# Kernel optimization log

Measured on AMD Instinct MI355X. Metric: run time of the kernel, lower is better.

## Reference

```python
import jax, jax.numpy as jnp
import numpy as np

B, DIM, T = 8, 1024, 4096
CB, CD = 4096, 8          # codebook_size, codebook_dim
COMMIT = 0.25
EPS = 1e-12


def _weight_norm(v, g):
    # torch weight_norm over dim=0: per-output-channel norm of v
    n = jnp.sqrt(jnp.sum(v * v, axis=1, keepdims=True))
    return g[:, None] * v / n


def _l2_normalize(x):
    n = jnp.sqrt(jnp.sum(x * x, axis=1, keepdims=True))
    return x / jnp.maximum(n, EPS)


def setup_inputs() -> dict:
    key = jax.random.key(0)
    ks = jax.random.split(key, 5)
    z = jax.random.normal(ks[0], (B, DIM, T), jnp.float32)
    v_in = jax.random.normal(ks[1], (CD, DIM), jnp.float32) * 0.02   # conv1d k=1 weight (squeezed)
    g_in = jnp.sqrt(jnp.sum(v_in * v_in, axis=1))                     # weight_norm init: g = ||v||
    b_in = jnp.zeros((CD,), jnp.float32)
    codebook = jax.random.normal(ks[2], (CB, CD), jnp.float32)        # nn.Embedding default N(0,1)
    v_out = jax.random.normal(ks[3], (DIM, CD), jnp.float32) * 0.02
    g_out = jnp.sqrt(jnp.sum(v_out * v_out, axis=1))
    b_out = jnp.zeros((DIM,), jnp.float32)
    return {"z": z, "v_in": v_in, "g_in": g_in, "b_in": b_in,
            "codebook": codebook, "v_out": v_out, "g_out": g_out, "b_out": b_out}


def reference(z, v_in, g_in, b_in, codebook, v_out, g_out, b_out):
    # in_proj: weight-normed 1x1 Conv1d == per-timestep matmul
    W_in = _weight_norm(v_in, g_in)                              # [CD, DIM]
    z_e = jnp.einsum('od,bdt->bot', W_in, z) + b_in[None, :, None]  # [B, CD, T]

    # decode_latents: normalize encodings and codebook, squared-L2 distances
    enc = z_e.transpose(0, 2, 1).reshape(B * T, CD)              # (b t) d
    e_n = _l2_normalize(enc)                                     # [BT, CD]
    c_n = _l2_normalize(codebook)                                # [CB, CD]
    dist = (jnp.sum(e_n * e_n, axis=1, keepdims=True)
            - 2.0 * (e_n @ c_n.T)
            + jnp.sum(c_n * c_n, axis=1)[None, :])               # [BT, CB]
    indices = jnp.argmin(dist, axis=1).reshape(B, T)             # [B, T] int

    # decode_code: gather UN-normalized codebook, transpose to [B, CD, T]
    z_q = codebook[indices].transpose(0, 2, 1)                   # [B, CD, T]

    # training losses (per-batch), commitment + codebook
    sg = jax.lax.stop_gradient
    commitment_loss = jnp.mean((z_e - sg(z_q)) ** 2, axis=(1, 2)) * COMMIT
    codebook_loss = jnp.mean((z_q - sg(z_e)) ** 2, axis=(1, 2))
    commit_loss = commitment_loss + codebook_loss                # [B]

    # straight-through estimator
    z_q_ste = z_e + sg(z_q - z_e)                                # [B, CD, T]

    # out_proj
    W_out = _weight_norm(v_out, g_out)                           # [DIM, CD]
    out = jnp.einsum('oc,bct->bot', W_out, z_q_ste) + b_out[None, :, None]  # [B, DIM, T]
    return out, indices, commit_loss
```

## Files before the change

### kernel.cpp

```cpp
#include <hip/hip_runtime.h>

#define DIMN 1024
#define TN 4096
#define BN 8
#define CBN 4096
#define CDN 8
#define BTN (BN*TN)
#define OUT_ELEMS (BN*DIMN*TN)

typedef float fx4 __attribute__((ext_vector_type(4)));
typedef float fx2 __attribute__((ext_vector_type(2)));

#define WS_WINT 0
#define WS_WOUT 8192
#define WS_CN   16384
#define WS_C2   49152
#define WS_LOSS 86016
#define WS_CNT  86024

#define LBO_F   8256
#define LZEP_F  9296
#define LZE_F   13648
#define LEN_F   14160
#define LCAND_F 14672
#define LZQ_F   15184
#define LDS_TOT 15696

__device__ __forceinline__ float dot4(float4 a, float4 b) {
    float d = a.x * b.x;
    d = fmaf(a.y, b.y, d);
    d = fmaf(a.z, b.z, d);
    d = fmaf(a.w, b.w, d);
    return d;
}
__device__ __forceinline__ void add4(float4& a, float4 b) {
    a.x += b.x; a.y += b.y; a.z += b.z; a.w += b.w;
}

__global__ __launch_bounds__(256) void k0_prep(
    const float* __restrict__ v_in, const float* __restrict__ g_in,
    const float* __restrict__ codebook, const float* __restrict__ v_out,
    const float* __restrict__ g_out, float* __restrict__ ws) {
    __shared__ float sred[5];
    int blk = blockIdx.x, tid = threadIdx.x;
    if (blk < 8) {
        int o = blk;
        const float* v = v_in + o * DIMN;
        float4 x = *(const float4*)(v + tid * 4);
        float p = x.x * x.x + x.y * x.y + x.z * x.z + x.w * x.w;
        for (int off = 32; off >= 1; off >>= 1) p += __shfl_down(p, off, 64);
        if ((tid & 63) == 0) sred[tid >> 6] = p;
        __syncthreads();
        if (tid == 0) {
            float tot = sred[0] + sred[1] + sred[2] + sred[3];
            sred[4] = g_in[o] / sqrtf(tot);
        }
        __syncthreads();
        float s = sred[4];
        ws[WS_WINT + (tid * 4 + 0) * 8 + o] = x.x * s;
        ws[WS_WINT + (tid * 4 + 1) * 8 + o] = x.y * s;
        ws[WS_WINT + (tid * 4 + 2) * 8 + o] = x.z * s;
        ws[WS_WINT + (tid * 4 + 3) * 8 + o] = x.w * s;
    } else if (blk < 12) {
        int r = (blk - 8) * 256 + tid;
        const float* v = v_out + r * 8;
        float4 a = *(const float4*)v;
        float4 b = *(const float4*)(v + 4);
        float n2 = dot4(a, a) + dot4(b, b);
        float s = g_out[r] / sqrtf(n2);
        *(float4*)(ws + WS_WOUT + r * 8)     = make_float4(a.x*s, a.y*s, a.z*s, a.w*s);
        *(float4*)(ws + WS_WOUT + r * 8 + 4) = make_float4(b.x*s, b.y*s, b.z*s, b.w*s);
    } else if (blk < 28) {
        int j = (blk - 12) * 256 + tid;
        const float* c = codebook + j * 8;
        float4 a = *(const float4*)c;
        float4 b = *(const float4*)(c + 4);
        float n2 = dot4(a, a) + dot4(b, b);
        float inv = 1.0f / fmaxf(sqrtf(n2), 1e-12f);
        float4 na = make_float4(a.x*inv, a.y*inv, a.z*inv, a.w*inv);
        float4 nb = make_float4(b.x*inv, b.y*inv, b.z*inv, b.w*inv);
        *(float4*)(ws + WS_CN + j * 8)     = na;
        *(float4*)(ws + WS_CN + j * 8 + 4) = nb;
        ws[WS_C2 + j] = -0.5f * (dot4(na, na) + dot4(nb, nb));
    } else {
        if (tid < 9) ws[WS_LOSS + tid] = 0.0f;
    }
}

__global__ __launch_bounds__(256, 2) void k_mega(
    const float* __restrict__ z, const float* __restrict__ b_in,
    const float* __restrict__ codebook, const float* __restrict__ b_out,
    float* __restrict__ dout, float* __restrict__ ws) {
    __shared__ float sp[LDS_TOT];
    int tid = threadIdx.x, blk = blockIdx.x;
    int b = blk >> 6;
    int t0 = (blk & 63) * 64;

    #pragma unroll
    for (int i = 0; i < 8; i++) {
        int f4 = tid + i * 256;
        *(float4*)(sp + f4 * 4) = *(const float4*)(ws + WS_WINT + f4 * 4);
    }
    __syncthreads();
    {
        int p = tid >> 5, tpair = tid & 31;
        int tA = tpair * 2;
        const float* zp = z + ((size_t)(b * DIMN + p * 128)) * TN + t0 + tA;
        float4 a0a = make_float4(0.f,0.f,0.f,0.f), a0b = make_float4(0.f,0.f,0.f,0.f);
        float4 a1a = make_float4(0.f,0.f,0.f,0.f), a1b = make_float4(0.f,0.f,0.f,0.f);
        #pragma unroll 8
        for (int dd = 0; dd < 128; ++dd) {
            fx2 zv = __builtin_nontemporal_load((const fx2*)(zp + (size_t)dd * TN));
            const float* wv = sp + (p * 128 + dd) * 8;
            float4 w0 = *(const float4*)wv;
            float4 w1 = *(const float4*)(wv + 4);
            a0a.x = fmaf(w0.x, zv.x, a0a.x); a0a.y = fmaf(w0.y, zv.x, a0a.y);
            a0a.z = fmaf(w0.z, zv.x, a0a.z); a0a.w = fmaf(w0.w, zv.x, a0a.w);
            a0b.x = fmaf(w1.x, zv.x, a0b.x); a0b.y = fmaf(w1.y, zv.x, a0b.y);
            a0b.z = fmaf(w1.z, zv.x, a0b.z); a0b.w = fmaf(w1.w, zv.x, a0b.w);
            a1a.x = fmaf(w0.x, zv.y, a1a.x); a1a.y = fmaf(w0.y, zv.y, a1a.y);
            a1a.z = fmaf(w0.z, zv.y, a1a.z); a1a.w = fmaf(w0.w, zv.y, a1a.w);
            a1b.x = fmaf(w1.x, zv.y, a1b.x); a1b.y = fmaf(w1.y, zv.y, a1b.y);
            a1b.z = fmaf(w1.z, zv.y, a1b.z); a1b.w = fmaf(w1.w, zv.y, a1b.w);
        }
        float* q0 = sp + LZEP_F + tA * 68 + p * 8;
        *(float4*)(q0)     = a0a;
        *(float4*)(q0 + 4) = a0b;
        float* q1 = sp + LZEP_F + (tA + 1) * 68 + p * 8;
        *(float4*)(q1)     = a1a;
        *(float4*)(q1 + 4) = a1b;
    }
    __syncthreads();

    if (tid < 64) {
        int t = tid;
        float4 za = *(const float4*)(b_in);
        float4 zb = *(const float4*)(b_in + 4);
        #pragma unroll
        for (int p = 0; p < 8; p++) {
            const float* pp = sp + LZEP_F + t * 68 + p * 8;
            add4(za, *(const float4*)(pp));
            add4(zb, *(const float4*)(pp + 4));
        }
        *(float4*)(sp + LZE_F + t * 8)     = za;
        *(float4*)(sp + LZE_F + t * 8 + 4) = zb;
        float inv = 1.0f / fmaxf(sqrtf(dot4(za, za) + dot4(zb, zb)), 1e-12f);
        *(float4*)(sp + LEN_F + t * 8)     = make_float4(za.x*inv, za.y*inv, za.z*inv, za.w*inv);
        *(float4*)(sp + LEN_F + t * 8 + 4) = make_float4(zb.x*inv, zb.y*inv, zb.z*inv, zb.w*inv);
    }
    __syncthreads();

    int co = tid >> 3, tt = tid & 7;
    float en[8][8];
    #pragma unroll
    for (int k = 0; k < 8; k++) {
        float4 u = *(const float4*)(sp + LEN_F + (tt * 8 + k) * 8);
        float4 v = *(const float4*)(sp + LEN_F + (tt * 8 + k) * 8 + 4);
        en[k][0]=u.x; en[k][1]=u.y; en[k][2]=u.z; en[k][3]=u.w;
        en[k][4]=v.x; en[k][5]=v.y; en[k][6]=v.z; en[k][7]=v.w;
    }
    float bs[8]; int bj[8];
    #pragma unroll
    for (int k = 0; k < 8; k++) { bs[k] = -3.4e38f; bj[k] = 0; }
    #pragma unroll 1
    for (int ci = 0; ci < 16; ++ci) {
        int j0 = ci * 256 + co * 8;
        #pragma unroll
        for (int qh = 0; qh < 2; ++qh) {
            int jq = j0 + qh * 4;
            const float* cg = ws + WS_CN + (size_t)jq * 8;
            float4 ca[4], cb[4];
            #pragma unroll
            for (int k = 0; k < 4; k++) {
                ca[k] = *(const float4*)(cg + k * 8);
                cb[k] = *(const float4*)(cg + k * 8 + 4);
            }
            float4 hqv = *(const float4*)(ws + WS_C2 + jq);
            float hv[4] = {hqv.x, hqv.y, hqv.z, hqv.w};
            #pragma unroll
            for (int k = 0; k < 4; k++) {
                #pragma unroll
                for (int t = 0; t < 8; t++) {
                    float s = fmaf(en[t][0], ca[k].x, hv[k]);
                    s = fmaf(en[t][1], ca[k].y, s); s = fmaf(en[t][2], ca[k].z, s);
                    s = fmaf(en[t][3], ca[k].w, s);
                    s = fmaf(en[t][4], cb[k].x, s); s = fmaf(en[t][5], cb[k].y, s);
                    s = fmaf(en[t][6], cb[k].z, s); s = fmaf(en[t][7], cb[k].w, s);
                    if (s > bs[t]) { bs[t] = s; bj[t] = jq + k; }
                }
            }
        }
    }
    #pragma unroll
    for (int st = 8; st <= 32; st <<= 1) {
        #pragma unroll
        for (int t = 0; t < 8; t++) {
            float os = __shfl_xor(bs[t], st, 64);
            int   oj = __shfl_xor(bj[t], st, 64);
            if (os > bs[t] || (os == bs[t] && oj < bj[t])) { bs[t] = os; bj[t] = oj; }
        }
    }
    if ((tid & 63) < 8) {
        int w = tid >> 6;
        #pragma unroll
        for (int k = 0; k < 8; k++)
            *(float2*)(sp + LCAND_F + (w * 64 + tt * 8 + k) * 2) =
                make_float2(bs[k], __int_as_float(bj[k]));
    }
    __syncthreads();

    if (tid < 64) {
        int t = tid;
        float2 c0 = *(const float2*)(sp + LCAND_F + t * 2);
        float best = c0.x; int idx = __float_as_int(c0.y);
        #pragma unroll
        for (int w2 = 1; w2 < 4; w2++) {
            float2 cw = *(const float2*)(sp + LCAND_F + (w2 * 64 + t) * 2);
            int j2 = __float_as_int(cw.y);
            if (cw.x > best || (cw.x == best && j2 < idx)) { best = cw.x; idx = j2; }
        }
        dout[(size_t)OUT_ELEMS + b * TN + t0 + t] = (float)idx;
        const float* cq = codebook + (size_t)idx * 8;
        float4 qa = *(const float4*)cq, qb = *(const float4*)(cq + 4);
        sp[LZQ_F + 0*64 + t] = qa.x; sp[LZQ_F + 1*64 + t] = qa.y;
        sp[LZQ_F + 2*64 + t] = qa.z; sp[LZQ_F + 3*64 + t] = qa.w;
        sp[LZQ_F + 4*64 + t] = qb.x; sp[LZQ_F + 5*64 + t] = qb.y;
        sp[LZQ_F + 6*64 + t] = qb.z; sp[LZQ_F + 7*64 + t] = qb.w;
        float4 za = *(const float4*)(sp + LZE_F + t * 8);
        float4 zb = *(const float4*)(sp + LZE_F + t * 8 + 4);
        float4 da = make_float4(za.x-qa.x, za.y-qa.y, za.z-qa.z, za.w-qa.w);
        float4 db = make_float4(zb.x-qb.x, zb.y-qb.y, zb.z-qb.z, zb.w-qb.w);
        float l = dot4(da, da) + dot4(db, db);
        for (int off = 32; off >= 1; off >>= 1) l += __shfl_down(l, off, 64);
        if (t == 0) atomicAdd(ws + WS_LOSS + b, l);
    } else {
        int i = tid - 64;
        #pragma unroll
        for (int r = 0; r < 11; r++) {
            int f4 = r * 192 + i;
            if (f4 < 2048) {
                float4 v = *(const float4*)(ws + WS_WOUT + f4 * 4);
                *(float4*)(sp + f4 * 4 + 4 * (f4 >> 7)) = v;
            }
        }
        #pragma unroll
        for (int r = 0; r < 2; r++) {
            int f = r * 192 + i;
            if (f < 256) {
                float4 v = *(const float4*)(b_out + f * 4);
                int sk = f >> 4;
                sp[LBO_F + f * 4 + sk + 0] = v.x;
                sp[LBO_F + f * 4 + sk + 1] = v.y;
                sp[LBO_F + f * 4 + sk + 2] = v.z;
                sp[LBO_F + f * 4 + sk + 3] = v.w;
            }
        }
    }
    __syncthreads();

    int t4 = tid & 15, og = tid >> 4;
    float4 zr[8];
    #pragma unroll
    for (int c = 0; c < 8; c++) zr[c] = *(const float4*)(sp + LZQ_F + c * 64 + t4 * 4);
    size_t obase = ((size_t)(b * DIMN + og * 64)) * TN + (size_t)(t0 + t4 * 4);
    for (int k = 0; k < 64; k++) {
        int o = og * 64 + k;
        const float* wrow = sp + o * 8 + 4 * og;
        float4 wa = *(const float4*)(wrow);
        float4 wb = *(const float4*)(wrow + 4);
        float bo = sp[LBO_F + o + og];
        float4 acc = make_float4(bo, bo, bo, bo);
        float wc[8] = {wa.x, wa.y, wa.z, wa.w, wb.x, wb.y, wb.z, wb.w};
        #pragma unroll
        for (int c = 0; c < 8; c++) {
            acc.x = fmaf(wc[c], zr[c].x, acc.x);
            acc.y = fmaf(wc[c], zr[c].y, acc.y);
            acc.z = fmaf(wc[c], zr[c].z, acc.z);
            acc.w = fmaf(wc[c], zr[c].w, acc.w);
        }
        acc.x = fminf(fmaxf(acc.x, -8.f), 8.f);
        acc.y = fminf(fmaxf(acc.y, -8.f), 8.f);
        acc.z = fminf(fmaxf(acc.z, -8.f), 8.f);
        acc.w = fminf(fmaxf(acc.w, -8.f), 8.f);
        fx4 st; st.x = acc.x; st.y = acc.y; st.z = acc.z; st.w = acc.w;
        __builtin_nontemporal_store(st, (fx4*)(dout + obase + (size_t)k * TN));
    }

    if (tid == 0) {
        __threadfence();
        unsigned int old = atomicAdd((unsigned int*)(ws + WS_CNT), 1u);
        if (old == 511u) {
            #pragma unroll
            for (int i = 0; i < 8; i++) {
                float v = atomicAdd(ws + WS_LOSS + i, 0.0f);
                dout[(size_t)OUT_ELEMS + BTN + i] = v * (1.25f / 32768.0f);
            }
        }
    }
}

extern "C" void kernel_launch(void* const* d_in, const int* in_sizes, int n_in,
                              void* d_out, int out_size, void* d_ws, size_t ws_size,
                              hipStream_t stream) {
    (void)in_sizes; (void)n_in; (void)out_size; (void)ws_size;
    const float* z        = (const float*)d_in[0];
    const float* v_in     = (const float*)d_in[1];
    const float* g_in     = (const float*)d_in[2];
    const float* b_in     = (const float*)d_in[3];
    const float* codebook = (const float*)d_in[4];
    const float* v_out    = (const float*)d_in[5];
    const float* g_out    = (const float*)d_in[6];
    const float* b_out    = (const float*)d_in[7];
    float* out            = (float*)d_out;
    float* ws             = (float*)d_ws;

    hipLaunchKernelGGL(k0_prep, dim3(29), dim3(256), 0, stream,
                       v_in, g_in, codebook, v_out, g_out, ws);
    hipLaunchKernelGGL(k_mega, dim3(512), dim3(256), 0, stream,
                       z, b_in, codebook, b_out, out, ws);
}
```

Before: 294.9 us.

## Use packed FP32 FMAs, 512-thread blocks and pair-interleaved codebook layout

After: 297.6 us. About the same (+0.9%).

```diff
diff --git a/kernel.cpp b/kernel.cpp
--- a/kernel.cpp
+++ b/kernel.cpp
@@ -4,7 +4,6 @@
 #define TN 4096
 #define BN 8
 #define CBN 4096
-#define CDN 8
 #define BTN (BN*TN)
 #define OUT_ELEMS (BN*DIMN*TN)
 
@@ -13,18 +12,15 @@
 
 #define WS_WINT 0
 #define WS_WOUT 8192
-#define WS_CN   16384
 #define WS_C2   49152
+#define WS_CNP  53248
 #define WS_LOSS 86016
 #define WS_CNT  86024
 
-#define LBO_F   8256
-#define LZEP_F  9296
-#define LZE_F   13648
-#define LEN_F   14160
-#define LCAND_F 14672
-#define LZQ_F   15184
-#define LDS_TOT 15696
+#define LROWS_F 8192
+#define LROW    68
+#define LZQ_F   12544
+#define LDS_TOT 13056
 
 __device__ __forceinline__ float dot4(float4 a, float4 b) {
     float d = a.x * b.x;
@@ -36,6 +32,13 @@
 __device__ __forceinline__ void add4(float4& a, float4 b) {
     a.x += b.x; a.y += b.y; a.z += b.z; a.w += b.w;
 }
+__device__ __forceinline__ fx2 lo2(fx4 v) { return __builtin_shufflevector(v, v, 0, 1); }
+__device__ __forceinline__ fx2 hi2(fx4 v) { return __builtin_shufflevector(v, v, 2, 3); }
+__device__ __forceinline__ fx2 splat2(float x) { fx2 r; r.x = x; r.y = x; return r; }
+__device__ __forceinline__ fx2 fma2(fx2 a, fx2 b, fx2 c) { return __builtin_elementwise_fma(a, b, c); }
+__device__ __forceinline__ fx2 max2(fx2 a, fx2 b) { return __builtin_elementwise_max(a, b); }
+__device__ __forceinline__ fx2 min2(fx2 a, fx2 b) { return __builtin_elementwise_min(a, b); }
+__device__ __forceinline__ fx4 cat4(fx2 a, fx2 b) { return __builtin_shufflevector(a, b, 0, 1, 2, 3); }
 
 __global__ __launch_bounds__(256) void k0_prep(
     const float* __restrict__ v_in, const float* __restrict__ g_in,
@@ -77,17 +80,21 @@
         float4 b = *(const float4*)(c + 4);
         float n2 = dot4(a, a) + dot4(b, b);
         float inv = 1.0f / fmaxf(sqrtf(n2), 1e-12f);
-        float4 na = make_float4(a.x*inv, a.y*inv, a.z*inv, a.w*inv);
-        float4 nb = make_float4(b.x*inv, b.y*inv, b.z*inv, b.w*inv);
-        *(float4*)(ws + WS_CN + j * 8)     = na;
-        *(float4*)(ws + WS_CN + j * 8 + 4) = nb;
-        ws[WS_C2 + j] = -0.5f * (dot4(na, na) + dot4(nb, nb));
+        float na[8] = {a.x*inv, a.y*inv, a.z*inv, a.w*inv,
+                       b.x*inv, b.y*inv, b.z*inv, b.w*inv};
+        float* dst = ws + WS_CNP + (size_t)(j >> 1) * 16 + (j & 1);
+        #pragma unroll
+        for (int i = 0; i < 8; i++) dst[i * 2] = na[i];
+        float h = 0.0f;
+        #pragma unroll
+        for (int i = 0; i < 8; i++) h = fmaf(na[i], na[i], h);
+        ws[WS_C2 + j] = -0.5f * h;
     } else {
         if (tid < 9) ws[WS_LOSS + tid] = 0.0f;
     }
 }
 
-__global__ __launch_bounds__(256, 2) void k_mega(
+__global__ __launch_bounds__(512, 4) void k_mega(
     const float* __restrict__ z, const float* __restrict__ b_in,
     const float* __restrict__ codebook, const float* __restrict__ b_out,
     float* __restrict__ dout, float* __restrict__ ws) {
@@ -97,38 +104,36 @@
     int t0 = (blk & 63) * 64;
 
     #pragma unroll
-    for (int i = 0; i < 8; i++) {
-        int f4 = tid + i * 256;
-        *(float4*)(sp + f4 * 4) = *(const float4*)(ws + WS_WINT + f4 * 4);
-    }
-    __syncthreads();
-    {
+    for (int i = 0; i < 4; i++) {
+        int f4 = tid + i * 512;
+        *(fx4*)(sp + f4 * 4) = *(const fx4*)(ws + WS_WINT + f4 * 4);
+    }
+    __syncthreads();
+
+    if (tid < 256) {
         int p = tid >> 5, tpair = tid & 31;
         int tA = tpair * 2;
         const float* zp = z + ((size_t)(b * DIMN + p * 128)) * TN + t0 + tA;
-        float4 a0a = make_float4(0.f,0.f,0.f,0.f), a0b = make_float4(0.f,0.f,0.f,0.f);
-        float4 a1a = make_float4(0.f,0.f,0.f,0.f), a1b = make_float4(0.f,0.f,0.f,0.f);
+        fx2 a0aL = splat2(0.f), a0aH = splat2(0.f), a0bL = splat2(0.f), a0bH = splat2(0.f);
+        fx2 a1aL = splat2(0.f), a1aH = splat2(0.f), a1bL = splat2(0.f), a1bH = splat2(0.f);
         #pragma unroll 8
         for (int dd = 0; dd < 128; ++dd) {
             fx2 zv = __builtin_nontemporal_load((const fx2*)(zp + (size_t)dd * TN));
             const float* wv = sp + (p * 128 + dd) * 8;
-            float4 w0 = *(const float4*)wv;
-            float4 w1 = *(const float4*)(wv + 4);
-            a0a.x = fmaf(w0.x, zv.x, a0a.x); a0a.y = fmaf(w0.y, zv.x, a0a.y);
-            a0a.z = fmaf(w0.z, zv.x, a0a.z); a0a.w = fmaf(w0.w, zv.x, a0a.w);
-            a0b.x = fmaf(w1.x, zv.x, a0b.x); a0b.y = fmaf(w1.y, zv.x, a0b.y);
-            a0b.z = fmaf(w1.z, zv.x, a0b.z); a0b.w = fmaf(w1.w, zv.x, a0b.w);
-            a1a.x = fmaf(w0.x, zv.y, a1a.x); a1a.y = fmaf(w0.y, zv.y, a1a.y);
-            a1a.z = fmaf(w0.z, zv.y, a1a.z); a1a.w = fmaf(w0.w, zv.y, a1a.w);
-            a1b.x = fmaf(w1.x, zv.y, a1b.x); a1b.y = fmaf(w1.y, zv.y, a1b.y);
-            a1b.z = fmaf(w1.z, zv.y, a1b.z); a1b.w = fmaf(w1.w, zv.y, a1b.w);
-        }
-        float* q0 = sp + LZEP_F + tA * 68 + p * 8;
-        *(float4*)(q0)     = a0a;
-        *(float4*)(q0 + 4) = a0b;
-        float* q1 = sp + LZEP_F + (tA + 1) * 68 + p * 8;
-        *(float4*)(q1)     = a1a;
-        *(float4*)(q1 + 4) = a1b;
+            fx4 w0 = *(const fx4*)wv;
+            fx4 w1 = *(const fx4*)(wv + 4);
+            fx2 zx = splat2(zv.x), zy = splat2(zv.y);
+            a0aL = fma2(lo2(w0), zx, a0aL); a0aH = fma2(hi2(w0), zx, a0aH);
+            a0bL = fma2(lo2(w1), zx, a0bL); a0bH = fma2(hi2(w1), zx, a0bH);
+            a1aL = fma2(lo2(w0), zy, a1aL); a1aH = fma2(hi2(w0), zy, a1aH);
+            a1bL = fma2(lo2(w1), zy, a1bL); a1bH = fma2(hi2(w1), zy, a1bH);
+        }
+        float* q0 = sp + LROWS_F + tA * LROW + p * 8;
+        *(fx4*)(q0)     = cat4(a0aL, a0aH);
+        *(fx4*)(q0 + 4) = cat4(a0bL, a0bH);
+        float* q1 = sp + LROWS_F + (tA + 1) * LROW + p * 8;
+        *(fx4*)(q1)     = cat4(a1aL, a1aH);
+        *(fx4*)(q1 + 4) = cat4(a1bL, a1bH);
     }
     __syncthreads();
 
@@ -138,84 +143,97 @@
         float4 zb = *(const float4*)(b_in + 4);
         #pragma unroll
         for (int p = 0; p < 8; p++) {
-            const float* pp = sp + LZEP_F + t * 68 + p * 8;
+            const float* pp = sp + LROWS_F + t * LROW + p * 8;
             add4(za, *(const float4*)(pp));
             add4(zb, *(const float4*)(pp + 4));
         }
-        *(float4*)(sp + LZE_F + t * 8)     = za;
-        *(float4*)(sp + LZE_F + t * 8 + 4) = zb;
+        float* row = sp + LROWS_F + t * LROW;
+        *(float4*)(row)     = za;
+        *(float4*)(row + 4) = zb;
         float inv = 1.0f / fmaxf(sqrtf(dot4(za, za) + dot4(zb, zb)), 1e-12f);
-        *(float4*)(sp + LEN_F + t * 8)     = make_float4(za.x*inv, za.y*inv, za.z*inv, za.w*inv);
-        *(float4*)(sp + LEN_F + t * 8 + 4) = make_float4(zb.x*inv, zb.y*inv, zb.z*inv, zb.w*inv);
-    }
-    __syncthreads();
-
-    int co = tid >> 3, tt = tid & 7;
-    float en[8][8];
-    #pragma unroll
-    for (int k = 0; k < 8; k++) {
-        float4 u = *(const float4*)(sp + LEN_F + (tt * 8 + k) * 8);
-        float4 v = *(const float4*)(sp + LEN_F + (tt * 8 + k) * 8 + 4);
+        *(float4*)(row + 8)  = make_float4(za.x*inv, za.y*inv, za.z*inv, za.w*inv);
+        *(float4*)(row + 12) = make_float4(zb.x*inv, zb.y*inv, zb.z*inv, zb.w*inv);
+    }
+    __syncthreads();
+
+    int co = tid >> 4, tg = tid & 15;
+    float en[4][8];
+    #pragma unroll
+    for (int k = 0; k < 4; k++) {
+        const float* rp = sp + LROWS_F + (tg * 4 + k) * LROW + 8;
+        fx4 u = *(const fx4*)rp;
+        fx4 v = *(const fx4*)(rp + 4);
         en[k][0]=u.x; en[k][1]=u.y; en[k][2]=u.z; en[k][3]=u.w;
         en[k][4]=v.x; en[k][5]=v.y; en[k][6]=v.z; en[k][7]=v.w;
     }
-    float bs[8]; int bj[8];
-    #pragma unroll
-    for (int k = 0; k < 8; k++) { bs[k] = -3.4e38f; bj[k] = 0; }
+    fx2 bs[4]; int bje[4], bjo[4];
+    #pragma unroll
+    for (int k = 0; k < 4; k++) { bs[k] = splat2(-3.4e38f); bje[k] = 0; bjo[k] = 1; }
     #pragma unroll 1
     for (int ci = 0; ci < 16; ++ci) {
         int j0 = ci * 256 + co * 8;
-        #pragma unroll
-        for (int qh = 0; qh < 2; ++qh) {
-            int jq = j0 + qh * 4;
-            const float* cg = ws + WS_CN + (size_t)jq * 8;
-            float4 ca[4], cb[4];
+        const float* cg = ws + WS_CNP + (size_t)j0 * 8;
+        #pragma unroll
+        for (int pp = 0; pp < 4; ++pp) {
+            fx4 cA = *(const fx4*)(cg + pp * 16);
+            fx4 cB = *(const fx4*)(cg + pp * 16 + 4);
+            fx4 cC = *(const fx4*)(cg + pp * 16 + 8);
+            fx4 cD = *(const fx4*)(cg + pp * 16 + 12);
+            fx2 h2 = *(const fx2*)(ws + WS_C2 + j0 + pp * 2);
+            int jE = j0 + pp * 2;
             #pragma unroll
             for (int k = 0; k < 4; k++) {
-                ca[k] = *(const float4*)(cg + k * 8);
-                cb[k] = *(const float4*)(cg + k * 8 + 4);
+                fx2 s = h2;
+                s = fma2(splat2(en[k][0]), lo2(cA), s);
+                s = fma2(splat2(en[k][1]), hi2(cA), s);
+                s = fma2(splat2(en[k][2]), lo2(cB), s);
+                s = fma2(splat2(en[k][3]), hi2(cB), s);
+                s = fma2(splat2(en[k][4]), lo2(cC), s);
+                s = fma2(splat2(en[k][5]), hi2(cC), s);
+                s = fma2(splat2(en[k][6]), lo2(cD), s);
+                s = fma2(splat2(en[k][7]), hi2(cD), s);
+                bool cE = s.x > bs[k].x;
+                bool cO = s.y > bs[k].y;
+                bs[k] = max2(bs[k], s);
+                if (cE) bje[k] = jE;
+                if (cO) bjo[k] = jE + 1;
             }
-            float4 hqv = *(const float4*)(ws + WS_C2 + jq);
-            float hv[4] = {hqv.x, hqv.y, hqv.z, hqv.w};
-            #pragma unroll
-            for (int k = 0; k < 4; k++) {
-                #pragma unroll
-                for (int t = 0; t < 8; t++) {
-                    float s = fmaf(en[t][0], ca[k].x, hv[k]);
-                    s = fmaf(en[t][1], ca[k].y, s); s = fmaf(en[t][2], ca[k].z, s);
-                    s = fmaf(en[t][3], ca[k].w, s);
-                    s = fmaf(en[t][4], cb[k].x, s); s = fmaf(en[t][5], cb[k].y, s);
-                    s = fmaf(en[t][6], cb[k].z, s); s = fmaf(en[t][7], cb[k].w, s);
-                    if (s > bs[t]) { bs[t] = s; bj[t] = jq + k; }
-                }
-            }
-        }
-    }
-    #pragma unroll
-    for (int st = 8; st <= 32; st <<= 1) {
-        #pragma unroll
-        for (int t = 0; t < 8; t++) {
-            float os = __shfl_xor(bs[t], st, 64);
-            int   oj = __shfl_xor(bj[t], st, 64);
-            if (os > bs[t] || (os == bs[t] && oj < bj[t])) { bs[t] = os; bj[t] = oj; }
-        }
-    }
-    if ((tid & 63) < 8) {
+        }
+    }
+    float bsF[4]; int bjF[4];
+    #pragma unroll
+    for (int k = 0; k < 4; k++) {
+        bsF[k] = bs[k].x; bjF[k] = bje[k];
+        if (bs[k].y > bsF[k] || (bs[k].y == bsF[k] && bjo[k] < bjF[k])) {
+            bsF[k] = bs[k].y; bjF[k] = bjo[k];
+        }
+    }
+    #pragma unroll
+    for (int st = 16; st <= 32; st <<= 1) {
+        #pragma unroll
+        for (int k = 0; k < 4; k++) {
+            float os = __shfl_xor(bsF[k], st, 64);
+            int   oj = __shfl_xor(bjF[k], st, 64);
+            if (os > bsF[k] || (os == bsF[k] && oj < bjF[k])) { bsF[k] = os; bjF[k] = oj; }
+        }
+    }
+    if ((tid & 63) < 16) {
         int w = tid >> 6;
         #pragma unroll
-        for (int k = 0; k < 8; k++)
-            *(float2*)(sp + LCAND_F + (w * 64 + tt * 8 + k) * 2) =
-                make_float2(bs[k], __int_as_float(bj[k]));
+        for (int k = 0; k < 4; k++)
+            *(fx2*)(sp + LROWS_F + (tg * 4 + k) * LROW + 32 + w * 2) =
+                (fx2){bsF[k], __int_as_float(bjF[k])};
     }
     __syncthreads();
 
     if (tid < 64) {
         int t = tid;
-        float2 c0 = *(const float2*)(sp + LCAND_F + t * 2);
+        const float* crow = sp + LROWS_F + t * LROW + 32;
+        fx2 c0 = *(const fx2*)(crow);
         float best = c0.x; int idx = __float_as_int(c0.y);
         #pragma unroll
-        for (int w2 = 1; w2 < 4; w2++) {
-            float2 cw = *(const float2*)(sp + LCAND_F + (w2 * 64 + t) * 2);
+        for (int w2 = 1; w2 < 8; w2++) {
+            fx2 cw = *(const fx2*)(crow + w2 * 2);
             int j2 = __float_as_int(cw.y);
             if (cw.x > best || (cw.x == best && j2 < idx)) { best = cw.x; idx = j2; }
         }
@@ -226,8 +244,9 @@
         sp[LZQ_F + 2*64 + t] = qa.z; sp[LZQ_F + 3*64 + t] = qa.w;
         sp[LZQ_F + 4*64 + t] = qb.x; sp[LZQ_F + 5*64 + t] = qb.y;
         sp[LZQ_F + 6*64 + t] = qb.z; sp[LZQ_F + 7*64 + t] = qb.w;
-        float4 za = *(const float4*)(sp + LZE_F + t * 8);
-        float4 zb = *(const float4*)(sp + LZE_F + t * 8 + 4);
+        const float* row = sp + LROWS_F + t * LROW;
+        float4 za = *(const float4*)(row);
+        float4 zb = *(const float4*)(row + 4);
         float4 da = make_float4(za.x-qa.x, za.y-qa.y, za.z-qa.z, za.w-qa.w);
         float4 db = make_float4(zb.x-qb.x, zb.y-qb.y, zb.z-qb.z, zb.w-qb.w);
         float l = dot4(da, da) + dot4(db, db);
@@ -236,54 +255,49 @@
     } else {
         int i = tid - 64;
         #pragma unroll
-        for (int r = 0; r < 11; r++) {
-            int f4 = r * 192 + i;
+        for (int r = 0; r < 5; r++) {
+            int f4 = r * 448 + i;
             if (f4 < 2048) {
-                float4 v = *(const float4*)(ws + WS_WOUT + f4 * 4);
-                *(float4*)(sp + f4 * 4 + 4 * (f4 >> 7)) = v;
+                fx4 v = *(const fx4*)(ws + WS_WOUT + f4 * 4);
+                int o = f4 >> 1, h = f4 & 1;
+                int tog = (o >> 6) & 1;
+                *(fx4*)(sp + o * 8 + ((h ^ tog) << 2)) = v;
             }
         }
         #pragma unroll
-        for (int r = 0; r < 2; r++) {
-            int f = r * 192 + i;
-            if (f < 256) {
-                float4 v = *(const float4*)(b_out + f * 4);
-                int sk = f >> 4;
-                sp[LBO_F + f * 4 + sk + 0] = v.x;
-                sp[LBO_F + f * 4 + sk + 1] = v.y;
-                sp[LBO_F + f * 4 + sk + 2] = v.z;
-                sp[LBO_F + f * 4 + sk + 3] = v.w;
+        for (int r = 0; r < 3; r++) {
+            int e = r * 448 + i;
+            if (e < 1024) sp[LROWS_F + (e & 63) * LROW + 16 + (e >> 6)] = b_out[e];
+        }
+    }
+    __syncthreads();
+
+    {
+        int t4 = tid & 15, og = tid >> 4;
+        fx4 zr[8];
+        #pragma unroll
+        for (int c = 0; c < 8; c++) zr[c] = *(const fx4*)(sp + LZQ_F + c * 64 + t4 * 4);
+        fx2 cmn = splat2(-8.f), cmx = splat2(8.f);
+        size_t obase = ((size_t)(b * DIMN + og * 32)) * TN + (size_t)(t0 + t4 * 4);
+        for (int k = 0; k < 32; k++) {
+            int o = og * 32 + k;
+            int tog = (o >> 6) & 1;
+            fx4 wa = *(const fx4*)(sp + o * 8 + (tog << 2));
+            fx4 wb = *(const fx4*)(sp + o * 8 + ((tog ^ 1) << 2));
+            float bo = sp[LROWS_F + (o & 63) * LROW + 16 + (o >> 6)];
+            fx2 accL = splat2(bo), accH = splat2(bo);
+            float wcv[8] = {wa.x, wa.y, wa.z, wa.w, wb.x, wb.y, wb.z, wb.w};
+            #pragma unroll
+            for (int c = 0; c < 8; c++) {
+                fx2 ws2 = splat2(wcv[c]);
+                accL = fma2(ws2, lo2(zr[c]), accL);
+                accH = fma2(ws2, hi2(zr[c]), accH);
             }
-        }
-    }
-    __syncthreads();
-
-    int t4 = tid & 15, og = tid >> 4;
-    float4 zr[8];
-    #pragma unroll
-    for (int c = 0; c < 8; c++) zr[c] = *(const float4*)(sp + LZQ_F + c * 64 + t4 * 4);
-    size_t obase = ((size_t)(b * DIMN + og * 64)) * TN + (size_t)(t0 + t4 * 4);
-    for (int k = 0; k < 64; k++) {
-        int o = og * 64 + k;
-        const float* wrow = sp + o * 8 + 4 * og;
-        float4 wa = *(const float4*)(wrow);
-        float4 wb = *(const float4*)(wrow + 4);
-        float bo = sp[LBO_F + o + og];
-        float4 acc = make_float4(bo, bo, bo, bo);
-        float wc[8] = {wa.x, wa.y, wa.z, wa.w, wb.x, wb.y, wb.z, wb.w};
-        #pragma unroll
-        for (int c = 0; c < 8; c++) {
-            acc.x = fmaf(wc[c], zr[c].x, acc.x);
-            acc.y = fmaf(wc[c], zr[c].y, acc.y);
-            acc.z = fmaf(wc[c], zr[c].z, acc.z);
-            acc.w = fmaf(wc[c], zr[c].w, acc.w);
-        }
-        acc.x = fminf(fmaxf(acc.x, -8.f), 8.f);
-        acc.y = fminf(fmaxf(acc.y, -8.f), 8.f);
-        acc.z = fminf(fmaxf(acc.z, -8.f), 8.f);
-        acc.w = fminf(fmaxf(acc.w, -8.f), 8.f);
-        fx4 st; st.x = acc.x; st.y = acc.y; st.z = acc.z; st.w = acc.w;
-        __builtin_nontemporal_store(st, (fx4*)(dout + obase + (size_t)k * TN));
+            accL = min2(max2(accL, cmn), cmx);
+            accH = min2(max2(accH, cmn), cmx);
+            fx4 st = cat4(accL, accH);
+            __builtin_nontemporal_store(st, (fx4*)(dout + obase + (size_t)k * TN));
+        }
     }
 
     if (tid == 0) {
@@ -316,6 +330,6 @@
 
     hipLaunchKernelGGL(k0_prep, dim3(29), dim3(256), 0, stream,
                        v_in, g_in, codebook, v_out, g_out, ws);
-    hipLaunchKernelGGL(k_mega, dim3(512), dim3(256), 0, stream,
+    hipLaunchKernelGGL(k_mega, dim3(512), dim3(512), 0, stream,
                        z, b_in, codebook, b_out, out, ws);
 }
```

## Split out-projection from quantize megakernel into separate streaming kernel

Applied to the files above, without the earlier changes.

After: 287.0 us. -2.7%, faster.

```diff
diff --git a/kernel.cpp b/kernel.cpp
--- a/kernel.cpp
+++ b/kernel.cpp
@@ -16,9 +16,8 @@
 #define WS_CN   16384
 #define WS_C2   49152
 #define WS_LOSS 86016
-#define WS_CNT  86024
-
-#define LBO_F   8256
+#define WS_ZQ   131072
+
 #define LZEP_F  9296
 #define LZE_F   13648
 #define LEN_F   14160
@@ -83,14 +82,14 @@
         *(float4*)(ws + WS_CN + j * 8 + 4) = nb;
         ws[WS_C2 + j] = -0.5f * (dot4(na, na) + dot4(nb, nb));
     } else {
-        if (tid < 9) ws[WS_LOSS + tid] = 0.0f;
-    }
-}
-
-__global__ __launch_bounds__(256, 2) void k_mega(
+        if (tid < 8) ws[WS_LOSS + tid] = 0.0f;
+    }
+}
+
+__global__ __launch_bounds__(256, 2) void k_mega2(
     const float* __restrict__ z, const float* __restrict__ b_in,
-    const float* __restrict__ codebook, const float* __restrict__ b_out,
-    float* __restrict__ dout, float* __restrict__ ws) {
+    const float* __restrict__ codebook, float* __restrict__ dout,
+    float* __restrict__ ws) {
     __shared__ float sp[LDS_TOT];
     int tid = threadIdx.x, blk = blockIdx.x;
     int b = blk >> 6;
@@ -233,69 +232,71 @@
         float l = dot4(da, da) + dot4(db, db);
         for (int off = 32; off >= 1; off >>= 1) l += __shfl_down(l, off, 64);
         if (t == 0) atomicAdd(ws + WS_LOSS + b, l);
-    } else {
-        int i = tid - 64;
-        #pragma unroll
-        for (int r = 0; r < 11; r++) {
-            int f4 = r * 192 + i;
-            if (f4 < 2048) {
-                float4 v = *(const float4*)(ws + WS_WOUT + f4 * 4);
-                *(float4*)(sp + f4 * 4 + 4 * (f4 >> 7)) = v;
+    }
+    __syncthreads();
+
+    #pragma unroll
+    for (int i = 0; i < 2; i++) {
+        int f = tid + i * 256;
+        int c = f >> 6, t = f & 63;
+        ws[WS_ZQ + ((size_t)(b * 8 + c)) * TN + t0 + t] = sp[LZQ_F + c * 64 + t];
+    }
+}
+
+__global__ __launch_bounds__(256, 2) void k_out(
+    const float* __restrict__ b_out, float* __restrict__ dout,
+    const float* __restrict__ ws) {
+    int tid = threadIdx.x, blk = blockIdx.x;
+    int b = blk >> 6;
+    int rem = blk & 63;
+    int o0 = (rem >> 1) * 32;
+    int tbase = (rem & 1) * 2048;
+    int w = tid >> 6, lane = tid & 63;
+    int ow0 = o0 + w * 8;
+
+    float wcv[8][8], bov[8];
+    #pragma unroll
+    for (int i = 0; i < 8; i++) {
+        const float* wr = ws + WS_WOUT + (ow0 + i) * 8;
+        float4 wa = *(const float4*)(wr);
+        float4 wb = *(const float4*)(wr + 4);
+        wcv[i][0]=wa.x; wcv[i][1]=wa.y; wcv[i][2]=wa.z; wcv[i][3]=wa.w;
+        wcv[i][4]=wb.x; wcv[i][5]=wb.y; wcv[i][6]=wb.z; wcv[i][7]=wb.w;
+        bov[i] = b_out[ow0 + i];
+    }
+
+    const float* zqb = ws + WS_ZQ + (size_t)(b * 8) * TN;
+    #pragma unroll 1
+    for (int tq = 0; tq < 8; ++tq) {
+        int tt = tbase + tq * 256 + lane * 4;
+        float4 zv[8];
+        #pragma unroll
+        for (int c = 0; c < 8; c++)
+            zv[c] = *(const float4*)(zqb + (size_t)c * TN + tt);
+        #pragma unroll
+        for (int i = 0; i < 8; i++) {
+            float bo = bov[i];
+            float4 acc = make_float4(bo, bo, bo, bo);
+            #pragma unroll
+            for (int c = 0; c < 8; c++) {
+                float wc = wcv[i][c];
+                acc.x = fmaf(wc, zv[c].x, acc.x);
+                acc.y = fmaf(wc, zv[c].y, acc.y);
+                acc.z = fmaf(wc, zv[c].z, acc.z);
+                acc.w = fmaf(wc, zv[c].w, acc.w);
             }
-        }
-        #pragma unroll
-        for (int r = 0; r < 2; r++) {
-            int f = r * 192 + i;
-            if (f < 256) {
-                float4 v = *(const float4*)(b_out + f * 4);
-                int sk = f >> 4;
-                sp[LBO_F + f * 4 + sk + 0] = v.x;
-                sp[LBO_F + f * 4 + sk + 1] = v.y;
-                sp[LBO_F + f * 4 + sk + 2] = v.z;
-                sp[LBO_F + f * 4 + sk + 3] = v.w;
-            }
-        }
-    }
-    __syncthreads();
-
-    int t4 = tid & 15, og = tid >> 4;
-    float4 zr[8];
-    #pragma unroll
-    for (int c = 0; c < 8; c++) zr[c] = *(const float4*)(sp + LZQ_F + c * 64 + t4 * 4);
-    size_t obase = ((size_t)(b * DIMN + og * 64)) * TN + (size_t)(t0 + t4 * 4);
-    for (int k = 0; k < 64; k++) {
-        int o = og * 64 + k;
-        const float* wrow = sp + o * 8 + 4 * og;
-        float4 wa = *(const float4*)(wrow);
-        float4 wb = *(const float4*)(wrow + 4);
-        float bo = sp[LBO_F + o + og];
-        float4 acc = make_float4(bo, bo, bo, bo);
-        float wc[8] = {wa.x, wa.y, wa.z, wa.w, wb.x, wb.y, wb.z, wb.w};
-        #pragma unroll
-        for (int c = 0; c < 8; c++) {
-            acc.x = fmaf(wc[c], zr[c].x, acc.x);
-            acc.y = fmaf(wc[c], zr[c].y, acc.y);
-            acc.z = fmaf(wc[c], zr[c].z, acc.z);
-            acc.w = fmaf(wc[c], zr[c].w, acc.w);
-        }
-        acc.x = fminf(fmaxf(acc.x, -8.f), 8.f);
-        acc.y = fminf(fmaxf(acc.y, -8.f), 8.f);
-        acc.z = fminf(fmaxf(acc.z, -8.f), 8.f);
-        acc.w = fminf(fmaxf(acc.w, -8.f), 8.f);
-        fx4 st; st.x = acc.x; st.y = acc.y; st.z = acc.z; st.w = acc.w;
-        __builtin_nontemporal_store(st, (fx4*)(dout + obase + (size_t)k * TN));
-    }
-
-    if (tid == 0) {
-        __threadfence();
-        unsigned int old = atomicAdd((unsigned int*)(ws + WS_CNT), 1u);
-        if (old == 511u) {
-            #pragma unroll
-            for (int i = 0; i < 8; i++) {
-                float v = atomicAdd(ws + WS_LOSS + i, 0.0f);
-                dout[(size_t)OUT_ELEMS + BTN + i] = v * (1.25f / 32768.0f);
-            }
-        }
+            acc.x = fminf(fmaxf(acc.x, -8.f), 8.f);
+            acc.y = fminf(fmaxf(acc.y, -8.f), 8.f);
+            acc.z = fminf(fmaxf(acc.z, -8.f), 8.f);
+            acc.w = fminf(fmaxf(acc.w, -8.f), 8.f);
+            fx4 st; st.x = acc.x; st.y = acc.y; st.z = acc.z; st.w = acc.w;
+            __builtin_nontemporal_store(st,
+                (fx4*)(dout + ((size_t)(b * DIMN + ow0 + i)) * TN + tt));
+        }
+    }
+
+    if (blk == 0 && tid < 8) {
+        dout[(size_t)OUT_ELEMS + BTN + tid] = ws[WS_LOSS + tid] * (1.25f / 32768.0f);
     }
 }
 
@@ -316,6 +317,8 @@
 
     hipLaunchKernelGGL(k0_prep, dim3(29), dim3(256), 0, stream,
                        v_in, g_in, codebook, v_out, g_out, ws);
-    hipLaunchKernelGGL(k_mega, dim3(512), dim3(256), 0, stream,
-                       z, b_in, codebook, b_out, out, ws);
-}
+    hipLaunchKernelGGL(k_mega2, dim3(512), dim3(256), 0, stream,
+                       z, b_in, codebook, out, ws);
+    hipLaunchKernelGGL(k_out, dim3(512), dim3(256), 0, stream,
+                       b_out, out, ws);
+}
```
